# Kernel optimization log

Hardware: AMD Instinct MI355X
Metric: run time of the kernel (lower is better)

Reference implementation:

```python
import jax, jax.numpy as jnp
import numpy as np

NUM_HEADS = 8  # matches init_kwargs num_heads
LN_EPS = 1e-5  # torch.nn.LayerNorm default


def setup_inputs() -> dict:
    key = jax.random.key(0)
    ks = jax.random.split(key, 12)
    E, B, H, S = 16384, 16, 256, 32
    edge_features = jax.random.normal(ks[0], (E, H), jnp.float32)
    edge_coords = jax.random.normal(ks[1], (E, 3), jnp.float32)
    # sorted, equal-size segments (all graphs non-empty)
    batch = jnp.repeat(jnp.arange(B, dtype=jnp.int32), E // B)
    s_h = 1.0 / np.sqrt(H)
    s_sh = 1.0 / np.sqrt(S * H)
    seed_vectors = jax.random.normal(ks[2], (S, H), jnp.float32)
    # weights stored [in, out] (transposed vs torch nn.Linear)
    Wq = jax.random.normal(ks[3], (H, H), jnp.float32) * s_h
    Wk = jax.random.normal(ks[4], (H, H), jnp.float32) * s_h
    Wv = jax.random.normal(ks[5], (H, H), jnp.float32) * s_h
    Wo = jax.random.normal(ks[6], (H, H), jnp.float32) * s_h
    bo = jnp.zeros((H,), jnp.float32)
    ln_g = jnp.ones((H,), jnp.float32)
    ln_b = jnp.zeros((H,), jnp.float32)
    W1 = jax.random.normal(ks[7], (S * H, H), jnp.float32) * s_sh
    b1 = jnp.zeros((H,), jnp.float32)
    W2 = jax.random.normal(ks[8], (H, H), jnp.float32) * s_h
    b2 = jnp.zeros((H,), jnp.float32)
    return dict(edge_features=edge_features, edge_coords=edge_coords, batch=batch,
                seed_vectors=seed_vectors, Wq=Wq, Wk=Wk, Wv=Wv, Wo=Wo, bo=bo,
                ln_g=ln_g, ln_b=ln_b, W1=W1, b1=b1, W2=W2, b2=b2, num_graphs=B)


def reference(edge_features, edge_coords, batch, seed_vectors, Wq, Wk, Wv, Wo, bo,
              ln_g, ln_b, W1, b1, W2, b2, num_graphs):
    S, H = seed_vectors.shape
    nh = NUM_HEADS
    hd = H // nh
    q = (seed_vectors @ Wq).reshape(S, nh, hd)          # shared across graphs
    k = (edge_features @ Wk).reshape(-1, nh, hd)        # [E, nh, hd]
    v = (edge_features @ Wv).reshape(-1, nh, hd)
    scores = jnp.einsum('shd,ehd->esh', q, k) / np.sqrt(hd).astype(np.float32)
    # segment softmax over edges within each graph
    m = jax.lax.stop_gradient(jax.ops.segment_max(scores, batch, num_segments=num_graphs))
    num = jnp.exp(scores - m[batch])
    den = jax.ops.segment_sum(num, batch, num_segments=num_graphs)
    w = num / den[batch]                                # [E, S, nh]
    att = jax.ops.segment_sum(jnp.einsum('esh,ehd->eshd', w, v), batch,
                              num_segments=num_graphs)  # [B, S, nh, hd]
    att = att.reshape(num_graphs, S, H)                 # concat heads (head-major)
    y = seed_vectors[None, :, :] + att @ Wo + bo        # residual + out_proj
    mu = jnp.mean(y, axis=-1, keepdims=True)
    var = jnp.mean((y - mu) ** 2, axis=-1, keepdims=True)
    y = (y - mu) / jnp.sqrt(var + LN_EPS) * ln_g + ln_b
    flat = y.reshape(num_graphs, S * H)
    h1 = jax.nn.silu(flat @ W1 + b1)
    return h1 @ W2 + b2                                 # [B, H]
```

## Files before the change

kernel.cpp:

```cpp
#include <hip/hip_runtime.h>
#include <math.h>
#include <stdint.h>

#define E_EDGES 16384
#define H_DIM   256
#define S_SEEDS 32
#define NHEADS  8
#define HDIM    32
#define BGRAPHS 16
#define EPG     1024
#define NCHUNK  256
#define CPG     16
#define RSQRT_HD 0.17677669529663687f

typedef __attribute__((ext_vector_type(8))) short bf16x8;
typedef __attribute__((ext_vector_type(4))) float f32x4;

__device__ inline unsigned short f2bf(float x) {
    unsigned u = __float_as_uint(x);
    u += 0x7fff + ((u >> 16) & 1);
    return (unsigned short)(u >> 16);
}
__device__ inline float bf2f(unsigned int h) {
    return __uint_as_float((h & 0xffffu) << 16);
}
__device__ inline unsigned pack2(float a, float b) {
    return (unsigned)f2bf(a) | ((unsigned)f2bf(b) << 16);
}

__global__ __launch_bounds__(256) void k_wc(const float* __restrict__ Wv,
                                            const float* __restrict__ Wk,
                                            const float* __restrict__ Wq,
                                            const float* __restrict__ seed,
                                            unsigned short* __restrict__ WcT) {
    int j = blockIdx.x;
    int i = threadIdx.x;
    float val;
    if (j < H_DIM) {
        val = Wv[i * H_DIM + j];
    } else {
        int c = j - H_DIM;
        int h = c >> 5, s = c & 31;
        __shared__ float qp[8][33];
        __shared__ float qrow[HDIM];
        int d = i & 31, g = i >> 5;
        const float* wq = &Wq[(g * 32) * H_DIM + h * HDIM + d];
        const float* sd = &seed[s * H_DIM + g * 32];
        float p = 0.f;
        #pragma unroll
        for (int ii = 0; ii < 32; ++ii)
            p = fmaf(sd[ii], wq[(size_t)ii * H_DIM], p);
        qp[g][d] = p;
        __syncthreads();
        if (i < HDIM) {
            float qv = 0.f;
            #pragma unroll
            for (int g2 = 0; g2 < 8; ++g2) qv += qp[g2][i];
            qrow[i] = qv;
        }
        __syncthreads();
        const float* wk = &Wk[i * H_DIM + h * HDIM];
        float acc = 0.f;
        #pragma unroll
        for (int dd = 0; dd < HDIM; dd += 4) {
            float4 w = *(const float4*)&wk[dd];
            float4 qq = *(const float4*)&qrow[dd];
            acc = fmaf(w.x, qq.x, acc); acc = fmaf(w.y, qq.y, acc);
            acc = fmaf(w.z, qq.z, acc); acc = fmaf(w.w, qq.w, acc);
        }
        val = acc * RSQRT_HD;
    }
    WcT[j * H_DIM + i] = f2bf(val);
}

__global__ __launch_bounds__(256) void k_attn(const float* __restrict__ A,
                                              const unsigned short* __restrict__ WcT,
                                              float* __restrict__ outc,
                                              float* __restrict__ mg,
                                              float* __restrict__ sg) {
    __shared__ unsigned short As[64][264];
    __shared__ unsigned short Bs[2][128][40];
    __shared__ unsigned short Vt[256][72];
    __shared__ unsigned short Pt[128][72];
    __shared__ float smx[2][128];
    __shared__ float ssm[2][128];
    int tid = threadIdx.x;
    int chunk = blockIdx.x;
    int e0 = chunk * 64;
    int w = tid >> 6, lane = tid & 63;
    int lr = lane & 15, kg = lane >> 4;
    int wm = (w & 1) * 32, wn = (w >> 1) * 64;

    {
        int r = tid >> 2, sg4 = tid & 3;
        const float* ap = &A[(size_t)(e0 + r) * H_DIM + sg4 * 64];
        #pragma unroll
        for (int i = 0; i < 8; ++i) {
            float4 x = *(const float4*)&ap[i * 8];
            float4 y = *(const float4*)&ap[i * 8 + 4];
            uint4 o;
            o.x = pack2(x.x, x.y); o.y = pack2(x.z, x.w);
            o.z = pack2(y.x, y.y); o.w = pack2(y.z, y.w);
            *(uint4*)&As[r][sg4 * 64 + i * 8] = o;
        }
    }
    int brow = tid >> 1, bhalf = (tid & 1) * 16;
    f32x4 acc2[2][2][2] = {};
    uint4 pb0, pb1;
    {
        const unsigned short* bp = &WcT[(size_t)brow * H_DIM + bhalf];
        pb0 = *(const uint4*)bp; pb1 = *(const uint4*)(bp + 8);
    }
    #pragma unroll
    for (int nt = 0; nt < 4; ++nt) {
        f32x4 acc[2][4] = {};
        #pragma unroll
        for (int k = 0; k < 8; ++k) {
            *(uint4*)&Bs[k & 1][brow][bhalf]     = pb0;
            *(uint4*)&Bs[k & 1][brow][bhalf + 8] = pb1;
            __syncthreads();
            int nk = k + 1, nnt = nt;
            if (nk == 8) { nk = 0; nnt = nt + 1; }
            if (nnt < 4) {
                const unsigned short* bp =
                    &WcT[(size_t)(nnt * 128 + brow) * H_DIM + nk * 32 + bhalf];
                pb0 = *(const uint4*)bp; pb1 = *(const uint4*)(bp + 8);
            }
            bf16x8 af[2], bfv[4];
            #pragma unroll
            for (int mi = 0; mi < 2; ++mi)
                af[mi] = *(const bf16x8*)&As[wm + mi * 16 + lr][k * 32 + kg * 8];
            #pragma unroll
            for (int ni = 0; ni < 4; ++ni)
                bfv[ni] = *(const bf16x8*)&Bs[k & 1][wn + ni * 16 + lr][kg * 8];
            #pragma unroll
            for (int mi = 0; mi < 2; ++mi)
                #pragma unroll
                for (int ni = 0; ni < 4; ++ni)
                    acc[mi][ni] = __builtin_amdgcn_mfma_f32_16x16x32_bf16(
                        af[mi], bfv[ni], acc[mi][ni], 0, 0, 0);
        }
        if (nt < 2) {
            #pragma unroll
            for (int mi = 0; mi < 2; ++mi)
                #pragma unroll
                for (int ni = 0; ni < 4; ++ni)
                    #pragma unroll
                    for (int r = 0; r < 4; ++r)
                        Vt[nt * 128 + wn + ni * 16 + lr][wm + mi * 16 + kg * 4 + r] =
                            f2bf(acc[mi][ni][r]);
        } else {
            int st = nt - 2;
            float tmax[4];
            #pragma unroll
            for (int ni = 0; ni < 4; ++ni) {
                float m = -1e30f;
                #pragma unroll
                for (int mi = 0; mi < 2; ++mi)
                    #pragma unroll
                    for (int r = 0; r < 4; ++r) m = fmaxf(m, acc[mi][ni][r]);
                m = fmaxf(m, __shfl_xor(m, 16, 64));
                m = fmaxf(m, __shfl_xor(m, 32, 64));
                tmax[ni] = m;
            }
            if (kg == 0) {
                #pragma unroll
                for (int ni = 0; ni < 4; ++ni) smx[w & 1][wn + ni * 16 + lr] = tmax[ni];
            }
            __syncthreads();
            float tsum[4];
            #pragma unroll
            for (int ni = 0; ni < 4; ++ni) {
                int col = wn + ni * 16 + lr;
                float m = fmaxf(smx[0][col], smx[1][col]);
                float sv = 0.f;
                #pragma unroll
                for (int mi = 0; mi < 2; ++mi)
                    #pragma unroll
                    for (int r = 0; r < 4; ++r) {
                        float e_ = __expf(acc[mi][ni][r] - m);
                        unsigned short eb = f2bf(e_);
                        Pt[col][wm + mi * 16 + kg * 4 + r] = eb;
                        sv += bf2f(eb);
                    }
                sv += __shfl_xor(sv, 16, 64);
                sv += __shfl_xor(sv, 32, 64);
                tsum[ni] = sv;
            }
            if (kg == 0) {
                #pragma unroll
                for (int ni = 0; ni < 4; ++ni) ssm[w & 1][wn + ni * 16 + lr] = tsum[ni];
            }
            __syncthreads();
            if (tid < 128) {
                float m = fmaxf(smx[0][tid], smx[1][tid]);
                float sv = ssm[0][tid] + ssm[1][tid];
                mg[(size_t)chunk * H_DIM + st * 128 + tid] = m;
                sg[(size_t)chunk * H_DIM + st * 128 + tid] = sv;
            }
            #pragma unroll
            for (int ms = 0; ms < 2; ++ms)
                #pragma unroll
                for (int nd = 0; nd < 2; ++nd)
                    #pragma unroll
                    for (int kk = 0; kk < 2; ++kk) {
                        bf16x8 pa = *(const bf16x8*)
                            &Pt[w * 32 + ms * 16 + lr][kk * 32 + kg * 8];
                        bf16x8 vb = *(const bf16x8*)
                            &Vt[(st * 4 + w) * 32 + nd * 16 + lr][kk * 32 + kg * 8];
                        acc2[st][ms][nd] = __builtin_amdgcn_mfma_f32_16x16x32_bf16(
                            pa, vb, acc2[st][ms][nd], 0, 0, 0);
                    }
        }
    }
    #pragma unroll
    for (int st = 0; st < 2; ++st)
        #pragma unroll
        for (int ms = 0; ms < 2; ++ms)
            #pragma unroll
            for (int nd = 0; nd < 2; ++nd)
                #pragma unroll
                for (int r = 0; r < 4; ++r) {
                    int s_ = ms * 16 + kg * 4 + r;
                    int c_ = (st * 4 + w) * 32 + nd * 16 + lr;
                    outc[((size_t)chunk * 32 + s_) * H_DIM + c_] = acc2[st][ms][nd][r];
                }
}

__device__ inline float block_sum256(float v, float* red4) {
    for (int o = 32; o > 0; o >>= 1) v += __shfl_xor(v, o, 64);
    int wid = threadIdx.x >> 6;
    if ((threadIdx.x & 63) == 0) red4[wid] = v;
    __syncthreads();
    float r = red4[0] + red4[1] + red4[2] + red4[3];
    __syncthreads();
    return r;
}

__global__ __launch_bounds__(256) void k_proj_ln(const float* __restrict__ outc,
                                                 const float* __restrict__ mg,
                                                 const float* __restrict__ sg,
                                                 const float* __restrict__ seed,
                                                 const float* __restrict__ Wo,
                                                 const float* __restrict__ bo,
                                                 const float* __restrict__ ln_g,
                                                 const float* __restrict__ ln_b,
                                                 float* __restrict__ Y) {
    int bs0 = blockIdx.x * 4;
    int c = threadIdx.x;
    int b = bs0 >> 5;
    __shared__ float sscale[4][CPG][8];
    __shared__ float arow[4][H_DIM];
    __shared__ float red4[4];
    if (c < 32) {
        int r = c >> 3, hh = c & 7;
        int s_r = (bs0 + r) & 31;
        int sc = hh * 32 + s_r;
        float mj[CPG];
        float M = -1e30f;
        #pragma unroll
        for (int j = 0; j < CPG; ++j) {
            mj[j] = mg[(size_t)(b * CPG + j) * H_DIM + sc];
            M = fmaxf(M, mj[j]);
        }
        float Den = 0.f;
        #pragma unroll
        for (int j = 0; j < CPG; ++j)
            Den += sg[(size_t)(b * CPG + j) * H_DIM + sc] * __expf(mj[j] - M);
        float inv = 1.f / Den;
        #pragma unroll
        for (int j = 0; j < CPG; ++j)
            sscale[r][j][hh] = __expf(mj[j] - M) * inv;
    }
    __syncthreads();
    int h = c >> 5;
    #pragma unroll
    for (int r = 0; r < 4; ++r) {
        int s_r = (bs0 + r) & 31;
        float a = 0.f;
        #pragma unroll
        for (int j = 0; j < CPG; ++j)
            a = fmaf(outc[((size_t)(b * CPG + j) * 32 + s_r) * H_DIM + c],
                     sscale[r][j][h], a);
        arow[r][c] = a;
    }
    __syncthreads();
    float acc[4];
    float b0 = bo[c];
    #pragma unroll
    for (int r = 0; r < 4; ++r) acc[r] = b0;
    for (int i = 0; i < H_DIM; i += 4) {
        float4 a0 = *(const float4*)&arow[0][i];
        float4 a1 = *(const float4*)&arow[1][i];
        float4 a2 = *(const float4*)&arow[2][i];
        float4 a3 = *(const float4*)&arow[3][i];
        float w0 = Wo[(i + 0) * H_DIM + c], w1 = Wo[(i + 1) * H_DIM + c];
        float w2 = Wo[(i + 2) * H_DIM + c], w3 = Wo[(i + 3) * H_DIM + c];
        acc[0] = fmaf(a0.x, w0, acc[0]); acc[0] = fmaf(a0.y, w1, acc[0]);
        acc[0] = fmaf(a0.z, w2, acc[0]); acc[0] = fmaf(a0.w, w3, acc[0]);
        acc[1] = fmaf(a1.x, w0, acc[1]); acc[1] = fmaf(a1.y, w1, acc[1]);
        acc[1] = fmaf(a1.z, w2, acc[1]); acc[1] = fmaf(a1.w, w3, acc[1]);
        acc[2] = fmaf(a2.x, w0, acc[2]); acc[2] = fmaf(a2.y, w1, acc[2]);
        acc[2] = fmaf(a2.z, w2, acc[2]); acc[2] = fmaf(a2.w, w3, acc[2]);
        acc[3] = fmaf(a3.x, w0, acc[3]); acc[3] = fmaf(a3.y, w1, acc[3]);
        acc[3] = fmaf(a3.z, w2, acc[3]); acc[3] = fmaf(a3.w, w3, acc[3]);
    }
    float g = ln_g[c], be = ln_b[c];
    #pragma unroll
    for (int r = 0; r < 4; ++r) {
        int bs = bs0 + r;
        float y = seed[(bs & 31) * H_DIM + c] + acc[r];
        float mu = block_sum256(y, red4) * (1.f / 256.f);
        float d = y - mu;
        float var = block_sum256(d * d, red4) * (1.f / 256.f);
        Y[(size_t)bs * H_DIM + c] = d * rsqrtf(var + 1e-5f) * g + be;
    }
}

__global__ __launch_bounds__(256) void k_mlp1(const float* __restrict__ Y,
                                              const float* __restrict__ W1,
                                              float* __restrict__ part) {
    int ch = blockIdx.x;
    int c = threadIdx.x;
    int i0 = ch * 64;
    __shared__ float fbuf[16][64];
    #pragma unroll
    for (int it = 0; it < 4; ++it) {
        int li = it * 256 + c;
        fbuf[li >> 6][li & 63] = Y[(size_t)(li >> 6) * 8192 + i0 + (li & 63)];
    }
    __syncthreads();
    float acc[16];
    #pragma unroll
    for (int b = 0; b < 16; ++b) acc[b] = 0.f;
    for (int ii = 0; ii < 64; ++ii) {
        float w = W1[(size_t)(i0 + ii) * H_DIM + c];
        #pragma unroll
        for (int b = 0; b < 16; ++b) acc[b] = fmaf(fbuf[b][ii], w, acc[b]);
    }
    #pragma unroll
    for (int b = 0; b < 16; ++b)
        part[((size_t)b * 128 + ch) * H_DIM + c] = acc[b];
}

__global__ __launch_bounds__(256) void k_mlp2(const float* __restrict__ part,
                                              const float* __restrict__ b1,
                                              const float* __restrict__ W2,
                                              const float* __restrict__ b2,
                                              float* __restrict__ out) {
    int b = blockIdx.x;
    int c = threadIdx.x;
    float s = b1[c];
    const float* pb = &part[(size_t)b * 128 * H_DIM + c];
    #pragma unroll 4
    for (int ch = 0; ch < 128; ++ch) s += pb[(size_t)ch * H_DIM];
    float h1 = s / (1.f + __expf(-s));
    __shared__ float hrow[H_DIM];
    hrow[c] = h1;
    __syncthreads();
    float acc = b2[c];
    for (int j = 0; j < H_DIM; j += 4) {
        float4 hq = *(const float4*)&hrow[j];
        acc = fmaf(hq.x, W2[(j + 0) * H_DIM + c], acc);
        acc = fmaf(hq.y, W2[(j + 1) * H_DIM + c], acc);
        acc = fmaf(hq.z, W2[(j + 2) * H_DIM + c], acc);
        acc = fmaf(hq.w, W2[(j + 3) * H_DIM + c], acc);
    }
    out[(size_t)b * H_DIM + c] = acc;
}

extern "C" void kernel_launch(void* const* d_in, const int* in_sizes, int n_in,
                              void* d_out, int out_size, void* d_ws, size_t ws_size,
                              hipStream_t stream) {
    const float* edge_features = (const float*)d_in[0];
    const float* seed = (const float*)d_in[3];
    const float* Wq   = (const float*)d_in[4];
    const float* Wk   = (const float*)d_in[5];
    const float* Wv   = (const float*)d_in[6];
    const float* Wo   = (const float*)d_in[7];
    const float* bo   = (const float*)d_in[8];
    const float* ln_g = (const float*)d_in[9];
    const float* ln_b = (const float*)d_in[10];
    const float* W1   = (const float*)d_in[11];
    const float* b1   = (const float*)d_in[12];
    const float* W2   = (const float*)d_in[13];
    const float* b2   = (const float*)d_in[14];
    float* out = (float*)d_out;

    float* ws = (float*)d_ws;
    unsigned short* WcT = (unsigned short*)ws;
    float* outc = ws + 65536;
    float* mg   = outc + 2097152;
    float* sg   = mg + 65536;
    float* Y    = sg + 65536;
    float* part = Y + 131072;

    k_wc      <<<512, 256, 0, stream>>>(Wv, Wk, Wq, seed, WcT);
    k_attn    <<<NCHUNK, 256, 0, stream>>>(edge_features, WcT, outc, mg, sg);
    k_proj_ln <<<BGRAPHS * S_SEEDS / 4, 256, 0, stream>>>(outc, mg, sg, seed, Wo, bo, ln_g, ln_b, Y);
    k_mlp1    <<<128, 256, 0, stream>>>(Y, W1, part);
    k_mlp2    <<<BGRAPHS, 256, 0, stream>>>(part, b1, W2, b2, out);
}
```

Baseline: 152.8 us.

## Split attention block into two 256-thread halves processing head groups in parallel

The attention kernel now launches 512 threads per block, and each half of the block handles one half of the V and score columns (one group of four heads). The two halves run concurrently instead of looping over four column tiles serially. The B staging buffer and the P buffer share shared memory through a union, which keeps the LDS footprint bounded. This is meant to raise per-block parallelism and shorten the serial chain, since there are only 256 blocks. In exchange, every block-wide barrier now synchronizes twice as many waves.

```diff
diff --git a/kernel.cpp b/kernel.cpp
--- a/kernel.cpp
+++ b/kernel.cpp
@@ -73,66 +73,77 @@
     WcT[j * H_DIM + i] = f2bf(val);
 }
 
-__global__ __launch_bounds__(256) void k_attn(const float* __restrict__ A,
+struct HalfBuf {
+    union {
+        unsigned short Bs[2][128][40];
+        unsigned short Pt[128][72];
+    };
+};
+struct SMattn {
+    unsigned short As[64][264];
+    HalfBuf hb[2];
+    unsigned short Vt[2][128][72];
+    float smx[2][2][128];
+    float ssm[2][2][128];
+};
+
+__global__ __launch_bounds__(512) void k_attn(const float* __restrict__ A,
                                               const unsigned short* __restrict__ WcT,
                                               float* __restrict__ outc,
                                               float* __restrict__ mg,
                                               float* __restrict__ sg) {
-    __shared__ unsigned short As[64][264];
-    __shared__ unsigned short Bs[2][128][40];
-    __shared__ unsigned short Vt[256][72];
-    __shared__ unsigned short Pt[128][72];
-    __shared__ float smx[2][128];
-    __shared__ float ssm[2][128];
+    __shared__ SMattn sm;
     int tid = threadIdx.x;
     int chunk = blockIdx.x;
     int e0 = chunk * 64;
-    int w = tid >> 6, lane = tid & 63;
+    int half = tid >> 8;
+    int tl = tid & 255;
+    int w4 = tl >> 6, lane = tid & 63;
     int lr = lane & 15, kg = lane >> 4;
-    int wm = (w & 1) * 32, wn = (w >> 1) * 64;
+    int wm = (w4 & 1) * 32, wn = (w4 >> 1) * 64;
 
     {
-        int r = tid >> 2, sg4 = tid & 3;
-        const float* ap = &A[(size_t)(e0 + r) * H_DIM + sg4 * 64];
-        #pragma unroll
-        for (int i = 0; i < 8; ++i) {
+        int r = tid >> 3, cg8 = tid & 7;
+        const float* ap = &A[(size_t)(e0 + r) * H_DIM + cg8 * 32];
+        #pragma unroll
+        for (int i = 0; i < 4; ++i) {
             float4 x = *(const float4*)&ap[i * 8];
             float4 y = *(const float4*)&ap[i * 8 + 4];
             uint4 o;
             o.x = pack2(x.x, x.y); o.y = pack2(x.z, x.w);
             o.z = pack2(y.x, y.y); o.w = pack2(y.z, y.w);
-            *(uint4*)&As[r][sg4 * 64 + i * 8] = o;
-        }
-    }
-    int brow = tid >> 1, bhalf = (tid & 1) * 16;
-    f32x4 acc2[2][2][2] = {};
+            *(uint4*)&sm.As[r][cg8 * 32 + i * 8] = o;
+        }
+    }
+    int brow = tl >> 1, bhalf16 = (tl & 1) * 16;
+    f32x4 acc2[2][2] = {};
     uint4 pb0, pb1;
     {
-        const unsigned short* bp = &WcT[(size_t)brow * H_DIM + bhalf];
+        const unsigned short* bp = &WcT[(size_t)(half * 128 + brow) * H_DIM + bhalf16];
         pb0 = *(const uint4*)bp; pb1 = *(const uint4*)(bp + 8);
     }
     #pragma unroll
-    for (int nt = 0; nt < 4; ++nt) {
+    for (int t2 = 0; t2 < 2; ++t2) {
         f32x4 acc[2][4] = {};
         #pragma unroll
         for (int k = 0; k < 8; ++k) {
-            *(uint4*)&Bs[k & 1][brow][bhalf]     = pb0;
-            *(uint4*)&Bs[k & 1][brow][bhalf + 8] = pb1;
+            *(uint4*)&sm.hb[half].Bs[k & 1][brow][bhalf16]     = pb0;
+            *(uint4*)&sm.hb[half].Bs[k & 1][brow][bhalf16 + 8] = pb1;
             __syncthreads();
-            int nk = k + 1, nnt = nt;
-            if (nk == 8) { nk = 0; nnt = nt + 1; }
-            if (nnt < 4) {
+            int nk = k + 1, nt2 = t2;
+            if (nk == 8) { nk = 0; nt2 = t2 + 1; }
+            if (nt2 < 2) {
                 const unsigned short* bp =
-                    &WcT[(size_t)(nnt * 128 + brow) * H_DIM + nk * 32 + bhalf];
+                    &WcT[(size_t)(half * 128 + nt2 * 256 + brow) * H_DIM + nk * 32 + bhalf16];
                 pb0 = *(const uint4*)bp; pb1 = *(const uint4*)(bp + 8);
             }
             bf16x8 af[2], bfv[4];
             #pragma unroll
             for (int mi = 0; mi < 2; ++mi)
-                af[mi] = *(const bf16x8*)&As[wm + mi * 16 + lr][k * 32 + kg * 8];
+                af[mi] = *(const bf16x8*)&sm.As[wm + mi * 16 + lr][k * 32 + kg * 8];
             #pragma unroll
             for (int ni = 0; ni < 4; ++ni)
-                bfv[ni] = *(const bf16x8*)&Bs[k & 1][wn + ni * 16 + lr][kg * 8];
+                bfv[ni] = *(const bf16x8*)&sm.hb[half].Bs[k & 1][wn + ni * 16 + lr][kg * 8];
             #pragma unroll
             for (int mi = 0; mi < 2; ++mi)
                 #pragma unroll
@@ -140,17 +151,16 @@
                     acc[mi][ni] = __builtin_amdgcn_mfma_f32_16x16x32_bf16(
                         af[mi], bfv[ni], acc[mi][ni], 0, 0, 0);
         }
-        if (nt < 2) {
+        if (t2 == 0) {
             #pragma unroll
             for (int mi = 0; mi < 2; ++mi)
                 #pragma unroll
                 for (int ni = 0; ni < 4; ++ni)
                     #pragma unroll
                     for (int r = 0; r < 4; ++r)
-                        Vt[nt * 128 + wn + ni * 16 + lr][wm + mi * 16 + kg * 4 + r] =
+                        sm.Vt[half][wn + ni * 16 + lr][wm + mi * 16 + kg * 4 + r] =
                             f2bf(acc[mi][ni][r]);
         } else {
-            int st = nt - 2;
             float tmax[4];
             #pragma unroll
             for (int ni = 0; ni < 4; ++ni) {
@@ -165,14 +175,15 @@
             }
             if (kg == 0) {
                 #pragma unroll
-                for (int ni = 0; ni < 4; ++ni) smx[w & 1][wn + ni * 16 + lr] = tmax[ni];
+                for (int ni = 0; ni < 4; ++ni)
+                    sm.smx[half][w4 & 1][wn + ni * 16 + lr] = tmax[ni];
             }
             __syncthreads();
             float tsum[4];
             #pragma unroll
             for (int ni = 0; ni < 4; ++ni) {
                 int col = wn + ni * 16 + lr;
-                float m = fmaxf(smx[0][col], smx[1][col]);
+                float m = fmaxf(sm.smx[half][0][col], sm.smx[half][1][col]);
                 float sv = 0.f;
                 #pragma unroll
                 for (int mi = 0; mi < 2; ++mi)
@@ -180,7 +191,7 @@
                     for (int r = 0; r < 4; ++r) {
                         float e_ = __expf(acc[mi][ni][r] - m);
                         unsigned short eb = f2bf(e_);
-                        Pt[col][wm + mi * 16 + kg * 4 + r] = eb;
+                        sm.hb[half].Pt[col][wm + mi * 16 + kg * 4 + r] = eb;
                         sv += bf2f(eb);
                     }
                 sv += __shfl_xor(sv, 16, 64);
@@ -189,14 +200,15 @@
             }
             if (kg == 0) {
                 #pragma unroll
-                for (int ni = 0; ni < 4; ++ni) ssm[w & 1][wn + ni * 16 + lr] = tsum[ni];
+                for (int ni = 0; ni < 4; ++ni)
+                    sm.ssm[half][w4 & 1][wn + ni * 16 + lr] = tsum[ni];
             }
             __syncthreads();
-            if (tid < 128) {
-                float m = fmaxf(smx[0][tid], smx[1][tid]);
-                float sv = ssm[0][tid] + ssm[1][tid];
-                mg[(size_t)chunk * H_DIM + st * 128 + tid] = m;
-                sg[(size_t)chunk * H_DIM + st * 128 + tid] = sv;
+            if (tl < 128) {
+                float m = fmaxf(sm.smx[half][0][tl], sm.smx[half][1][tl]);
+                float sv = sm.ssm[half][0][tl] + sm.ssm[half][1][tl];
+                mg[(size_t)chunk * H_DIM + half * 128 + tl] = m;
+                sg[(size_t)chunk * H_DIM + half * 128 + tl] = sv;
             }
             #pragma unroll
             for (int ms = 0; ms < 2; ++ms)
@@ -205,26 +217,24 @@
                     #pragma unroll
                     for (int kk = 0; kk < 2; ++kk) {
                         bf16x8 pa = *(const bf16x8*)
-                            &Pt[w * 32 + ms * 16 + lr][kk * 32 + kg * 8];
+                            &sm.hb[half].Pt[w4 * 32 + ms * 16 + lr][kk * 32 + kg * 8];
                         bf16x8 vb = *(const bf16x8*)
-                            &Vt[(st * 4 + w) * 32 + nd * 16 + lr][kk * 32 + kg * 8];
-                        acc2[st][ms][nd] = __builtin_amdgcn_mfma_f32_16x16x32_bf16(
-                            pa, vb, acc2[st][ms][nd], 0, 0, 0);
+                            &sm.Vt[half][w4 * 32 + nd * 16 + lr][kk * 32 + kg * 8];
+                        acc2[ms][nd] = __builtin_amdgcn_mfma_f32_16x16x32_bf16(
+                            pa, vb, acc2[ms][nd], 0, 0, 0);
                     }
         }
     }
     #pragma unroll
-    for (int st = 0; st < 2; ++st)
-        #pragma unroll
-        for (int ms = 0; ms < 2; ++ms)
-            #pragma unroll
-            for (int nd = 0; nd < 2; ++nd)
-                #pragma unroll
-                for (int r = 0; r < 4; ++r) {
-                    int s_ = ms * 16 + kg * 4 + r;
-                    int c_ = (st * 4 + w) * 32 + nd * 16 + lr;
-                    outc[((size_t)chunk * 32 + s_) * H_DIM + c_] = acc2[st][ms][nd][r];
-                }
+    for (int ms = 0; ms < 2; ++ms)
+        #pragma unroll
+        for (int nd = 0; nd < 2; ++nd)
+            #pragma unroll
+            for (int r = 0; r < 4; ++r) {
+                int s_ = ms * 16 + kg * 4 + r;
+                int c_ = (half * 4 + w4) * 32 + nd * 16 + lr;
+                outc[((size_t)chunk * 32 + s_) * H_DIM + c_] = acc2[ms][nd][r];
+            }
 }
 
 __device__ inline float block_sum256(float v, float* red4) {
@@ -396,7 +406,7 @@
     float* part = Y + 131072;
 
     k_wc      <<<512, 256, 0, stream>>>(Wv, Wk, Wq, seed, WcT);
-    k_attn    <<<NCHUNK, 256, 0, stream>>>(edge_features, WcT, outc, mg, sg);
+    k_attn    <<<NCHUNK, 512, 0, stream>>>(edge_features, WcT, outc, mg, sg);
     k_proj_ln <<<BGRAPHS * S_SEEDS / 4, 256, 0, stream>>>(outc, mg, sg, seed, Wo, bo, ln_g, ln_b, Y);
     k_mlp1    <<<128, 256, 0, stream>>>(Y, W1, part);
     k_mlp2    <<<BGRAPHS, 256, 0, stream>>>(part, b1, W2, b2, out);
```

New measurement: 152.9 us. Within noise of the previous version (+0.0%).
